# Optimization experiments

Hardware: AMD Instinct MI355X
Metric: run time of the kernel (lower is better)

Reference implementation:

```python
import jax, jax.numpy as jnp
import numpy as np

D_MODEL, SEQ, D_HEAD, N_HEAD, D_MLP = 1024, 2048, 64, 16, 4096
BATCH = 2
LN_EPS = 1e-5


def layer_norm(x, gamma, beta):
    mu = jnp.mean(x, axis=-1, keepdims=True)
    var = jnp.mean(jnp.square(x - mu), axis=-1, keepdims=True)
    return (x - mu) * jax.lax.rsqrt(var + LN_EPS) * gamma + beta


def setup_inputs() -> dict:
    key = jax.random.key(0)
    ks = jax.random.split(key, 10)
    s = 1.0 / np.sqrt(D_MODEL)
    x = jax.random.normal(ks[0], (BATCH, SEQ, D_MODEL), dtype=jnp.float32)
    # per-head Q/K/V projections, stacked: [H, d_model, d_head]
    wq = jax.random.uniform(ks[1], (N_HEAD, D_MODEL, D_HEAD), jnp.float32, -s, s)
    wk = jax.random.uniform(ks[2], (N_HEAD, D_MODEL, D_HEAD), jnp.float32, -s, s)
    wv = jax.random.uniform(ks[3], (N_HEAD, D_MODEL, D_HEAD), jnp.float32, -s, s)
    wo = jax.random.uniform(ks[4], (N_HEAD * D_HEAD, D_MODEL), jnp.float32, -s, s)
    sm = 1.0 / np.sqrt(D_MLP)
    w_in = jax.random.uniform(ks[5], (D_MODEL, D_MLP), jnp.float32, -s, s)
    b_in = jax.random.uniform(ks[6], (D_MLP,), jnp.float32, -s, s)
    w_out = jax.random.uniform(ks[7], (D_MLP, D_MODEL), jnp.float32, -sm, sm)
    b_out = jax.random.uniform(ks[8], (D_MODEL,), jnp.float32, -sm, sm)
    g1 = jnp.ones((D_MODEL,), jnp.float32)
    bt1 = jnp.zeros((D_MODEL,), jnp.float32)
    g2 = jnp.ones((D_MODEL,), jnp.float32)
    bt2 = jnp.zeros((D_MODEL,), jnp.float32)
    return {"x": x, "wq": wq, "wk": wk, "wv": wv, "wo": wo,
            "w_in": w_in, "b_in": b_in, "w_out": w_out, "b_out": b_out,
            "g1": g1, "bt1": bt1, "g2": g2, "bt2": bt2}


def reference(x, wq, wk, wv, wo, w_in, b_in, w_out, b_out, g1, bt1, g2, bt2):
    B, S, D = x.shape
    # multi-head attention (all heads batched)
    q = jnp.einsum('bsd,hde->bhse', x, wq)  # [B,H,S,dh]
    k = jnp.einsum('bsd,hde->bhse', x, wk)
    v = jnp.einsum('bsd,hde->bhse', x, wv)
    scores = jnp.einsum('bhie,bhje->bhij', q, k) / np.sqrt(D_HEAD)
    causal = jnp.tril(jnp.ones((S, S), dtype=bool))
    scores = jnp.where(causal, scores, -jnp.inf)
    attn = jax.nn.softmax(scores, axis=-1)
    head_out = jnp.einsum('bhij,bhje->bhie', attn, v)  # [B,H,S,dh]
    # concat heads in order (head 0 first) -> [B,S,H*dh]
    head_out = jnp.transpose(head_out, (0, 2, 1, 3)).reshape(B, S, N_HEAD * D_HEAD)
    x = x + layer_norm(head_out @ wo, g1, bt1)
    mlp = jax.nn.relu(x @ w_in + b_in) @ w_out + b_out
    x = x + layer_norm(mlp, g2, bt2)
    return x
```

## Files before the change

kernel.cpp:

```cpp
#include <hip/hip_runtime.h>
#include <hip/hip_bf16.h>
#include <math.h>

#define DM 1024
#define SEQ 2048
#define DH 64
#define NH 16
#define DMLP 4096
#define BATCH 2
#define ROWS (BATCH*SEQ)

typedef __attribute__((ext_vector_type(4))) float f32x4;
typedef __attribute__((ext_vector_type(8))) short bf16x8;

__device__ __forceinline__ void gl2lds16(const __hip_bfloat16* g, __hip_bfloat16* l) {
  __builtin_amdgcn_global_load_lds(
      (const __attribute__((address_space(1))) void*)g,
      (__attribute__((address_space(3))) void*)l, 16, 0, 0);
}

__device__ __forceinline__ float bfu2f(unsigned short u) {
  union { unsigned int i; float f; } cvt;
  cvt.i = ((unsigned int)u) << 16;
  return cvt.f;
}

template<int K, int OUT_BF16, int BIAS, int RELU>
__global__ __launch_bounds__(512) void gemm256(
    const __hip_bfloat16* __restrict__ A,
    const __hip_bfloat16* __restrict__ BT,
    float* __restrict__ Cf,
    __hip_bfloat16* __restrict__ Cb,
    const float* __restrict__ bias,
    int N)
{
  constexpr int NT = K / 64;
  __shared__ __align__(16) __hip_bfloat16 As[2][16384];
  __shared__ __align__(16) __hip_bfloat16 Bs[2][16384];
  const int t    = threadIdx.x;
  const int wave = t >> 6;
  const int lane = t & 63;
  const int col  = lane & 15;
  const int quad = lane >> 4;
  const int m0 = blockIdx.x * 256;
  const int n0 = blockIdx.y * 256;
  const int wm = (wave >> 2) * 128;
  const int wn = (wave & 3) * 64;

  const int tr = t >> 3;
  const int tc = (t & 7) ^ (tr & 7);
  const __hip_bfloat16* gA = A  + (size_t)(m0 + tr) * K + tc * 8;
  const __hip_bfloat16* gB = BT + (size_t)(n0 + tr) * K + tc * 8;

  const int sw  = col & 7;
  const int ao0 = ((quad)     ^ sw) * 8;
  const int ao1 = ((4 + quad) ^ sw) * 8;

  f32x4 acc[8][4] = {};

#define STAGE_A(h, u) do {                                                     \
    gl2lds16(gA + (size_t)(h)*128*K + (u)*64,                                  \
             &As[(u)&1][(h)*8192 + wave*512]);                                 \
    gl2lds16(gA + (size_t)(h)*128*K + (u)*64 + (size_t)64*K,                   \
             &As[(u)&1][(h)*8192 + 4096 + wave*512]);                          \
  } while (0)
#define STAGE_B(h, u) do {                                                     \
    gl2lds16(gB + (size_t)(h)*128*K + (u)*64,                                  \
             &Bs[(u)&1][(h)*8192 + wave*512]);                                 \
    gl2lds16(gB + (size_t)(h)*128*K + (u)*64 + (size_t)64*K,                   \
             &Bs[(u)&1][(h)*8192 + 4096 + wave*512]);                          \
  } while (0)
#define LOAD_A(base) do { _Pragma("unroll")                                    \
    for (int i = 0; i < 4; ++i) {                                              \
      af[i][0] = *(const bf16x8*)(pA + (base) + i*1024 + ao0);                 \
      af[i][1] = *(const bf16x8*)(pA + (base) + i*1024 + ao1);                 \
    } } while (0)
#define LOAD_BX(arr, base) do { _Pragma("unroll")                              \
    for (int j = 0; j < 2; ++j) {                                              \
      arr[j][0] = *(const bf16x8*)(pB + (base) + j*1024 + ao0);                \
      arr[j][1] = *(const bf16x8*)(pB + (base) + j*1024 + ao1);                \
    } } while (0)
#define PHASE_TAIL(MB, NB, BARR) do {                                          \
    asm volatile("s_barrier" ::: "memory");                                    \
    asm volatile("s_waitcnt lgkmcnt(0)" ::: "memory");                         \
    __builtin_amdgcn_s_setprio(1);                                             \
    _Pragma("unroll")                                                          \
    for (int kk = 0; kk < 2; ++kk)                                             \
      _Pragma("unroll")                                                        \
      for (int i = 0; i < 4; ++i)                                              \
        _Pragma("unroll")                                                      \
        for (int j = 0; j < 2; ++j)                                            \
          acc[(MB)+i][(NB)+j] = __builtin_amdgcn_mfma_f32_16x16x32_bf16(       \
              af[i][kk], BARR[j][kk], acc[(MB)+i][(NB)+j], 0, 0, 0);           \
    __builtin_amdgcn_s_setprio(0);                                             \
    asm volatile("s_barrier" ::: "memory");                                    \
  } while (0)

  STAGE_A(0, 0); STAGE_B(0, 0); STAGE_A(1, 0); STAGE_B(1, 0);
  if (NT > 1) {
    STAGE_A(0, 1); STAGE_B(0, 1); STAGE_A(1, 1); STAGE_B(1, 1);
    asm volatile("s_waitcnt vmcnt(8)" ::: "memory");
  } else {
    asm volatile("s_waitcnt vmcnt(0)" ::: "memory");
  }
  asm volatile("s_barrier" ::: "memory");

  #pragma unroll 2
  for (int u = 0; u < NT; ++u) {
    const __hip_bfloat16* pA = As[u & 1] + (wm + col) * 64;
    const __hip_bfloat16* pB = Bs[u & 1] + (wn + col) * 64;
    const bool s2 = (u + 2 < NT);
    bf16x8 af[4][2], bl[2][2], bh[2][2];

    LOAD_A(0);
    LOAD_BX(bl, 0);
    PHASE_TAIL(0, 0, bl);

    LOAD_BX(bh, 2048);
    PHASE_TAIL(0, 2, bh);

    LOAD_A(4096);
    if (s2) { STAGE_B(0, u + 2); STAGE_B(1, u + 2); }
    PHASE_TAIL(4, 2, bh);

    if (s2) {
      STAGE_A(0, u + 2); STAGE_A(1, u + 2);
      asm volatile("s_waitcnt vmcnt(8)" ::: "memory");
    } else {
      asm volatile("s_waitcnt vmcnt(0)" ::: "memory");
    }
    PHASE_TAIL(4, 0, bl);
  }
#undef STAGE_A
#undef STAGE_B
#undef LOAD_A
#undef LOAD_BX
#undef PHASE_TAIL

  #pragma unroll
  for (int mi = 0; mi < 8; ++mi) {
    #pragma unroll
    for (int ni = 0; ni < 4; ++ni) {
      const int cn = n0 + wn + ni*16 + col;
      float bv = 0.f;
      if (BIAS) bv = bias[cn];
      #pragma unroll
      for (int r = 0; r < 4; ++r) {
        const int cm = m0 + wm + mi*16 + quad*4 + r;
        float v = acc[mi][ni][r];
        if (BIAS) v += bv;
        if (RELU) v = fmaxf(v, 0.f);
        if (OUT_BF16) Cb[(size_t)cm * N + cn] = __float2bfloat16(v);
        else          Cf[(size_t)cm * N + cn] = v;
      }
    }
  }
}

template<int KS>
__global__ __launch_bounds__(512) void gemm256x128(
    const __hip_bfloat16* __restrict__ A,
    const __hip_bfloat16* __restrict__ BT,
    float* __restrict__ Cf,
    int N, int K, long long zstride)
{
  constexpr int NT = KS / 64;
  static_assert(NT >= 2, "pipeline needs >=2 K-tiles");
  __shared__ __align__(16) __hip_bfloat16 As[2][16384];
  __shared__ __align__(16) __hip_bfloat16 Bs[2][8192];
  const int t    = threadIdx.x;
  const int wave = t >> 6;
  const int lane = t & 63;
  const int col  = lane & 15;
  const int quad = lane >> 4;
  const int m0 = blockIdx.x * 256;
  const int n0 = blockIdx.y * 128;
  const int kz = (int)blockIdx.z * KS;
  const int wm = (wave >> 1) * 64;
  const int wn = (wave & 1) * 64;

  const int tr = t >> 3;
  const int tc = (t & 7) ^ (tr & 7);
  const __hip_bfloat16* gA = A  + (size_t)(m0 + tr) * K + kz + tc * 8;
  const __hip_bfloat16* gB = BT + (size_t)(n0 + tr) * K + kz + tc * 8;

  const int sw  = col & 7;
  const int ao0 = ((quad)     ^ sw) * 8;
  const int ao1 = ((4 + quad) ^ sw) * 8;

  f32x4 acc[4][4] = {};

#define SA(u) do { _Pragma("unroll")                                           \
    for (int q = 0; q < 4; ++q)                                                \
      gl2lds16(gA + (size_t)(q*64)*K + (u)*64,                                 \
               &As[(u)&1][q*4096 + wave*512]);                                 \
  } while (0)
#define SB(u) do { _Pragma("unroll")                                           \
    for (int q = 0; q < 2; ++q)                                                \
      gl2lds16(gB + (size_t)(q*64)*K + (u)*64,                                 \
               &Bs[(u)&1][q*4096 + wave*512]);                                 \
  } while (0)

  SA(0); SB(0); SA(1);

  #pragma unroll 2
  for (int v = 0; v < NT; ++v) {
    const __hip_bfloat16* pA = As[v & 1] + (wm + col) * 64;
    const __hip_bfloat16* pB = Bs[v & 1] + (wn + col) * 64;
    bf16x8 af[4][2], bf[4][2];

    if (v + 1 < NT) {
      SB(v + 1);
      asm volatile("s_waitcnt vmcnt(6)" ::: "memory");
    } else {
      asm volatile("s_waitcnt vmcnt(0)" ::: "memory");
    }
    asm volatile("s_barrier" ::: "memory");
    #pragma unroll
    for (int i = 0; i < 4; ++i) {
      af[i][0] = *(const bf16x8*)(pA + i*1024 + ao0);
      af[i][1] = *(const bf16x8*)(pA + i*1024 + ao1);
    }
    #pragma unroll
    for (int j = 0; j < 2; ++j) {
      bf[j][0] = *(const bf16x8*)(pB + j*1024 + ao0);
      bf[j][1] = *(const bf16x8*)(pB + j*1024 + ao1);
    }
    asm volatile("s_waitcnt lgkmcnt(0)" ::: "memory");
    __builtin_amdgcn_s_setprio(1);
    #pragma unroll
    for (int kk = 0; kk < 2; ++kk)
      #pragma unroll
      for (int i = 0; i < 4; ++i)
        #pragma unroll
        for (int j = 0; j < 2; ++j)
          acc[i][j] = __builtin_amdgcn_mfma_f32_16x16x32_bf16(
              af[i][kk], bf[j][kk], acc[i][j], 0, 0, 0);
    __builtin_amdgcn_s_setprio(0);
    asm volatile("s_barrier" ::: "memory");

    if (v + 2 < NT) SA(v + 2);
    #pragma unroll
    for (int j = 2; j < 4; ++j) {
      bf[j][0] = *(const bf16x8*)(pB + j*1024 + ao0);
      bf[j][1] = *(const bf16x8*)(pB + j*1024 + ao1);
    }
    asm volatile("s_waitcnt lgkmcnt(0)" ::: "memory");
    __builtin_amdgcn_s_setprio(1);
    #pragma unroll
    for (int kk = 0; kk < 2; ++kk)
      #pragma unroll
      for (int i = 0; i < 4; ++i)
        #pragma unroll
        for (int j = 2; j < 4; ++j)
          acc[i][j] = __builtin_amdgcn_mfma_f32_16x16x32_bf16(
              af[i][kk], bf[j][kk], acc[i][j], 0, 0, 0);
    __builtin_amdgcn_s_setprio(0);
    asm volatile("s_barrier" ::: "memory");
  }
#undef SA
#undef SB

  float* Co = Cf + (size_t)blockIdx.z * zstride;
  #pragma unroll
  for (int i = 0; i < 4; ++i) {
    #pragma unroll
    for (int j = 0; j < 4; ++j) {
      const int cn = n0 + wn + j*16 + col;
      #pragma unroll
      for (int r = 0; r < 4; ++r) {
        const int cm = m0 + wm + i*16 + quad*4 + r;
        Co[(size_t)cm * N + cn] = acc[i][j][r];
      }
    }
  }
}

__global__ __launch_bounds__(256) void attn_kernel(
    const __hip_bfloat16* __restrict__ qkv,
    const __hip_bfloat16* __restrict__ vt,
    __hip_bfloat16* __restrict__ aout,
    __hip_bfloat16* __restrict__ opart,
    float* __restrict__ lpart)
{
  __shared__ __align__(16) __hip_bfloat16 Ks[2][64*64];
  __shared__ __align__(16) __hip_bfloat16 Vts[64*64];
  __shared__ __align__(16) __hip_bfloat16 Ps[4][16*64];

  const int bh = blockIdx.x, b = bh >> 4, h = bh & 15;
  const int t = threadIdx.x, wave = t >> 6, lane = t & 63;
  const int col = lane & 15, quad = lane >> 4;
  const float SC = 0.125f * 1.44269504f;

  const int r0  = t >> 3;
  const int cs0 = (t & 7) ^ (r0 & 7);
  const __hip_bfloat16* kbase = qkv + (size_t)b*SEQ*3072 + 1024 + h*64;
  const __hip_bfloat16* vbase = vt + (size_t)bh*64*SEQ;

#define KISSUE(j0, buf) do {                                                      \
    gl2lds16(kbase + (size_t)((j0) + r0)*3072      + cs0*8, &Ks[buf][wave*512]);  \
    gl2lds16(kbase + (size_t)((j0) + 32 + r0)*3072 + cs0*8, &Ks[buf][2048 + wave*512]); \
  } while (0)
#define VISSUE(j0) do {                                                           \
    gl2lds16(vbase + (size_t)r0*SEQ        + (j0) + cs0*8,  &Vts[wave*512]);      \
    gl2lds16(vbase + (size_t)(32 + r0)*SEQ + (j0) + cs0*8,  &Vts[2048 + wave*512]); \
  } while (0)

  const int y = (int)blockIdx.y;
  int c, tile;
  if (y < 32)      { c = 0; tile = 31 - y;  }
  else if (y < 56) { c = 1; tile = 63 - y;  }
  else if (y < 72) { c = 2; tile = 87 - y;  }
  else             { c = 3; tile = 103 - y; }
  const int jbeg = c * 8;
  const int jend = jbeg + min(8, tile + 1 - jbeg);

  const int i0 = tile * 64;
  const int i0w = i0 + wave*16;

  bf16x8 aq[2];
  #pragma unroll
  for (int kk = 0; kk < 2; kk++)
    aq[kk] = *(const bf16x8*)&qkv[((size_t)(b*SEQ + i0w + col))*3072 + h*64 + kk*32 + quad*8];

  f32x4 O[4] = {};
  float lsum[4] = {0.f, 0.f, 0.f, 0.f};

  KISSUE(jbeg * 64, 0);
  for (int jt = jbeg; jt < jend; jt++) {
    const int cur = (jt - jbeg) & 1;
    const int j0 = jt * 64;
    const bool pf = (jt + 1 < jend);
    asm volatile("s_barrier" ::: "memory");
    VISSUE(j0);
    if (pf) {
      KISSUE(j0 + 64, cur ^ 1);
      asm volatile("s_waitcnt vmcnt(4)" ::: "memory");
    } else {
      asm volatile("s_waitcnt vmcnt(2)" ::: "memory");
    }

    f32x4 S[4] = {};
    __builtin_amdgcn_s_setprio(1);
    #pragma unroll
    for (int kk = 0; kk < 2; kk++) {
      const int sl = ((kk*4 + quad) ^ (col & 7)) * 8;
      #pragma unroll
      for (int jl = 0; jl < 4; jl++) {
        bf16x8 bk = *(const bf16x8*)&Ks[cur][(jl*16 + col)*64 + sl];
        S[jl] = __builtin_amdgcn_mfma_f32_16x16x32_bf16(aq[kk], bk, S[jl], 0, 0, 0);
      }
    }
    __builtin_amdgcn_s_setprio(0);

    const bool diag = (jt == tile);
    #pragma unroll
    for (int r = 0; r < 4; r++) {
      const int row = quad*4 + r;
      const int ig = i0 + wave*16 + row;
      #pragma unroll
      for (int jl = 0; jl < 4; jl++) {
        float p = exp2f(S[jl][r] * SC);
        if (diag && (j0 + jl*16 + col > ig)) p = 0.f;
        lsum[r] += p;
        const int cc = jl*2 + (col >> 3);
        Ps[wave][row*64 + (cc ^ (row & 7))*8 + (col & 7)] = __float2bfloat16(p);
      }
    }

    if (pf) asm volatile("s_waitcnt vmcnt(2)" ::: "memory");
    else    asm volatile("s_waitcnt vmcnt(0)" ::: "memory");

    __builtin_amdgcn_s_setprio(1);
    #pragma unroll
    for (int kk = 0; kk < 2; kk++) {
      const int sl = ((kk*4 + quad) ^ (col & 7)) * 8;
      bf16x8 ap = *(const bf16x8*)&Ps[wave][col*64 + sl];
      #pragma unroll
      for (int et = 0; et < 4; et++) {
        bf16x8 bv = *(const bf16x8*)&Vts[(et*16 + col)*64 + sl];
        O[et] = __builtin_amdgcn_mfma_f32_16x16x32_bf16(ap, bv, O[et], 0, 0, 0);
      }
    }
    __builtin_amdgcn_s_setprio(0);
  }

  #pragma unroll
  for (int r = 0; r < 4; r++) {
    float s = lsum[r];
    s += __shfl_xor(s, 1);
    s += __shfl_xor(s, 2);
    s += __shfl_xor(s, 4);
    s += __shfl_xor(s, 8);
    const int m = b*SEQ + i0w + quad*4 + r;
    if (tile < 8) {
      const float inv = 1.f / s;
      #pragma unroll
      for (int et = 0; et < 4; et++)
        aout[(size_t)m*DM + h*64 + et*16 + col] = __float2bfloat16(O[et][r] * inv);
    } else {
      __hip_bfloat16* op = opart + ((size_t)c*ROWS + m)*DM + h*64;
      #pragma unroll
      for (int et = 0; et < 4; et++)
        op[et*16 + col] = __float2bfloat16(O[et][r]);
      if (col == 0) lpart[((size_t)c*ROWS + m)*16 + h] = s;
    }
  }
#undef KISSUE
#undef VISSUE
}

__global__ __launch_bounds__(256) void attn_finalize(
    const __hip_bfloat16* __restrict__ opart,
    const float* __restrict__ lpart,
    __hip_bfloat16* __restrict__ aout)
{
  const int y = blockIdx.x;
  const int b = y / 1536;
  const int rem = y % 1536;
  const int tile = 8 + (rem >> 6);
  const int rr = rem & 63;
  const int m = b*SEQ + tile*64 + rr;
  const int nch = (tile >> 3) + 1;
  const int tid = threadIdx.x;
  const int h = tid >> 4;
  float o0 = 0.f, o1 = 0.f, o2 = 0.f, o3 = 0.f, l = 0.f;
  for (int c = 0; c < nch; ++c) {
    const ushort4 v = ((const ushort4*)(opart + ((size_t)c*ROWS + m)*DM))[tid];
    o0 += bfu2f(v.x); o1 += bfu2f(v.y); o2 += bfu2f(v.z); o3 += bfu2f(v.w);
    l  += lpart[((size_t)c*ROWS + m)*16 + h];
  }
  const float inv = 1.f / l;
  __hip_bfloat16* p = aout + (size_t)m*DM + tid*4;
  p[0] = __float2bfloat16(o0 * inv);
  p[1] = __float2bfloat16(o1 * inv);
  p[2] = __float2bfloat16(o2 * inv);
  p[3] = __float2bfloat16(o3 * inv);
}

__global__ __launch_bounds__(256) void ln_res(
    const float* __restrict__ y0,
    const float* __restrict__ y1,
    const float* __restrict__ bias,
    const float* __restrict__ xres,
    float* __restrict__ xout,
    __hip_bfloat16* __restrict__ bout,
    const float* __restrict__ gamma,
    const float* __restrict__ beta)
{
  const int row = blockIdx.x;
  const int t = threadIdx.x;
  float4 v = ((const float4*)(y0 + (size_t)row*DM))[t];
  if (y1) {
    const float4 w = ((const float4*)(y1 + (size_t)row*DM))[t];
    v.x += w.x; v.y += w.y; v.z += w.z; v.w += w.w;
  }
  if (bias) {
    const float4 w = ((const float4*)bias)[t];
    v.x += w.x; v.y += w.y; v.z += w.z; v.w += w.w;
  }
  float s  = v.x + v.y + v.z + v.w;
  float sq = v.x*v.x + v.y*v.y + v.z*v.z + v.w*v.w;
  #pragma unroll
  for (int off = 32; off > 0; off >>= 1) {
    s  += __shfl_down(s, off);
    sq += __shfl_down(sq, off);
  }
  __shared__ float red[8];
  const int wave = t >> 6, lane = t & 63;
  if (lane == 0) { red[wave] = s; red[4 + wave] = sq; }
  __syncthreads();
  s  = red[0] + red[1] + red[2] + red[3];
  sq = red[4] + red[5] + red[6] + red[7];
  const float mu   = s * (1.f/DM);
  const float var  = sq * (1.f/DM) - mu*mu;
  const float rstd = rsqrtf(var + 1e-5f);
  const float4 g  = ((const float4*)gamma)[t];
  const float4 bt = ((const float4*)beta)[t];
  const float4 xr = ((const float4*)(xres + (size_t)row*DM))[t];
  float4 o;
  o.x = (v.x - mu)*rstd*g.x + bt.x + xr.x;
  o.y = (v.y - mu)*rstd*g.y + bt.y + xr.y;
  o.z = (v.z - mu)*rstd*g.z + bt.z + xr.z;
  o.w = (v.w - mu)*rstd*g.w + bt.w + xr.w;
  ((float4*)(xout + (size_t)row*DM))[t] = o;
  if (bout) {
    __hip_bfloat16* bp = bout + (size_t)row*DM + t*4;
    bp[0] = __float2bfloat16(o.x);
    bp[1] = __float2bfloat16(o.y);
    bp[2] = __float2bfloat16(o.z);
    bp[3] = __float2bfloat16(o.w);
  }
}

__global__ __launch_bounds__(256) void transpose_cvt(
    const float* __restrict__ src, __hip_bfloat16* __restrict__ dst,
    int K, int N, long long sz, long long dz)
{
  __shared__ float tile[32][33];
  const int z = blockIdx.z;
  const int k0 = blockIdx.y * 32, n0 = blockIdx.x * 32;
  const int tx = threadIdx.x & 31, ty = threadIdx.x >> 5;
  const float* s = src + (size_t)z*sz;
  __hip_bfloat16* d = dst + (size_t)z*dz;
  for (int i = ty; i < 32; i += 8)
    tile[i][tx] = s[(size_t)(k0+i)*N + n0 + tx];
  __syncthreads();
  for (int i = ty; i < 32; i += 8)
    d[(size_t)(n0+i)*K + k0 + tx] = __float2bfloat16(tile[tx][i]);
}

__global__ __launch_bounds__(256) void transpose_v(
    const __hip_bfloat16* __restrict__ qkv, __hip_bfloat16* __restrict__ vt)
{
  __shared__ __hip_bfloat16 tile[32][33];
  const int bh = blockIdx.z, b = bh >> 4, h = bh & 15;
  const int s0 = blockIdx.x * 32, e0 = blockIdx.y * 32;
  const int tx = threadIdx.x & 31, ty = threadIdx.x >> 5;
  for (int i = ty; i < 32; i += 8)
    tile[i][tx] = qkv[(size_t)(b*SEQ + s0+i)*3072 + 2048 + h*64 + e0 + tx];
  __syncthreads();
  for (int i = ty; i < 32; i += 8)
    vt[((size_t)bh*64 + e0+i)*SEQ + s0 + tx] = tile[tx][i];
}

__global__ __launch_bounds__(256) void cvt_bf16(
    const float* __restrict__ src, __hip_bfloat16* __restrict__ dst, int n4)
{
  const int i = blockIdx.x*256 + threadIdx.x;
  if (i < n4) {
    const float4 v = ((const float4*)src)[i];
    dst[i*4+0] = __float2bfloat16(v.x);
    dst[i*4+1] = __float2bfloat16(v.y);
    dst[i*4+2] = __float2bfloat16(v.z);
    dst[i*4+3] = __float2bfloat16(v.w);
  }
}

extern "C" void kernel_launch(void* const* d_in, const int* in_sizes, int n_in,
                              void* d_out, int out_size, void* d_ws, size_t ws_size,
                              hipStream_t stream)
{
  const float* x     = (const float*)d_in[0];
  const float* wq    = (const float*)d_in[1];
  const float* wk    = (const float*)d_in[2];
  const float* wv    = (const float*)d_in[3];
  const float* wo    = (const float*)d_in[4];
  const float* w_in  = (const float*)d_in[5];
  const float* b_in  = (const float*)d_in[6];
  const float* w_out = (const float*)d_in[7];
  const float* b_out = (const float*)d_in[8];
  const float* g1    = (const float*)d_in[9];
  const float* bt1   = (const float*)d_in[10];
  const float* g2    = (const float*)d_in[11];
  const float* bt2   = (const float*)d_in[12];
  float* out = (float*)d_out;

  char* ws = (char*)d_ws;
  __hip_bfloat16* xb     = (__hip_bfloat16*)(ws + 0);
  __hip_bfloat16* wqkvT  = (__hip_bfloat16*)(ws + 8388608);
  __hip_bfloat16* woT    = (__hip_bfloat16*)(ws + 14680064);
  __hip_bfloat16* w_inT  = (__hip_bfloat16*)(ws + 16777216);
  __hip_bfloat16* w_outT = (__hip_bfloat16*)(ws + 25165824);
  __hip_bfloat16* qkvb   = (__hip_bfloat16*)(ws + 33554432);
  __hip_bfloat16* vtb    = (__hip_bfloat16*)(ws + 58720256);
  __hip_bfloat16* attn_o = (__hip_bfloat16*)(ws + 0);
  __hip_bfloat16* opart  = (__hip_bfloat16*)(ws + 67108864);
  float*          lpart  = (float*)(ws + 100663296);
  float*          P0     = (float*)(ws + 33554432);
  float*          x1     = (float*)(ws + 75497472);
  __hip_bfloat16* x1b    = (__hip_bfloat16*)(ws + 92274688);
  __hip_bfloat16* hbuf   = (__hip_bfloat16*)(ws + 33554432);
  float*          M0     = (float*)(ws + 0);
  float*          M1     = (float*)(ws + 100663296);
  float*          P1     = (float*)(ws + 50331648);

  const long long PROJ_ZS = (long long)ROWS * DM;
  const long long MLP_ZS  = 100663296LL / 4;

  cvt_bf16<<<ROWS*DM/4/256, 256, 0, stream>>>(x, xb, ROWS*DM/4);

  transpose_cvt<<<dim3(2,32,16), 256, 0, stream>>>(wq, wqkvT,             DM, DH, (long long)DM*DH, (long long)DH*DM);
  transpose_cvt<<<dim3(2,32,16), 256, 0, stream>>>(wk, wqkvT + 1024*1024, DM, DH, (long long)DM*DH, (long long)DH*DM);
  transpose_cvt<<<dim3(2,32,16), 256, 0, stream>>>(wv, wqkvT + 2048*1024, DM, DH, (long long)DM*DH, (long long)DH*DM);
  transpose_cvt<<<dim3(32,32,1),  256, 0, stream>>>(wo,    woT,    DM,   DM,   0, 0);
  transpose_cvt<<<dim3(128,32,1), 256, 0, stream>>>(w_in,  w_inT,  DM,   DMLP, 0, 0);
  transpose_cvt<<<dim3(32,128,1), 256, 0, stream>>>(w_out, w_outT, DMLP, DM,   0, 0);

  gemm256<DM,1,0,0><<<dim3(ROWS/256, 3072/256), 512, 0, stream>>>(xb, wqkvT, nullptr, qkvb, nullptr, 3072);
  transpose_v<<<dim3(SEQ/32, 2, BATCH*NH), 256, 0, stream>>>(qkvb, vtb);
  attn_kernel<<<dim3(BATCH*NH, 80), 256, 0, stream>>>(qkvb, vtb, attn_o, opart, lpart);
  attn_finalize<<<3072, 256, 0, stream>>>(opart, lpart, attn_o);
  gemm256x128<512><<<dim3(ROWS/256, DM/128, 2), 512, 0, stream>>>(attn_o, woT, P0, DM, DM, PROJ_ZS);
  ln_res<<<ROWS, 256, 0, stream>>>(P0, P1, nullptr, x, x1, x1b, g1, bt1);
  gemm256<DM,1,1,1><<<dim3(ROWS/256, DMLP/256), 512, 0, stream>>>(x1b, w_inT, nullptr, hbuf, b_in, DMLP);
  gemm256x128<2048><<<dim3(ROWS/256, DM/128, 2), 512, 0, stream>>>(hbuf, w_outT, M0, DM, DMLP, MLP_ZS);
  ln_res<<<ROWS, 256, 0, stream>>>(M0, M1, b_out, x1, out, nullptr, g2, bt2);
}
```

Before: 238.0 us.

## Double-buffer V tiles in attention, split diagonal masking, use native exp2/rcp

The V tile now gets its own double buffer in LDS and is prefetched one iteration ahead along with K, instead of being loaded at the start of each iteration. This takes the V global load latency off the critical path between the QK^T and PV MFMAs, and the second wait is no longer needed. The softmax loop is split into a masked diagonal path and an unmasked path, and uses the hardware exp2 and rcp intrinsics. The cost is more LDS, which may lower occupancy, and slightly less precise exp and reciprocal.

```diff
diff --git a/kernel.cpp b/kernel.cpp
--- a/kernel.cpp
+++ b/kernel.cpp
@@ -284,7 +284,7 @@
     float* __restrict__ lpart)
 {
   __shared__ __align__(16) __hip_bfloat16 Ks[2][64*64];
-  __shared__ __align__(16) __hip_bfloat16 Vts[64*64];
+  __shared__ __align__(16) __hip_bfloat16 Vts[2][64*64];
   __shared__ __align__(16) __hip_bfloat16 Ps[4][16*64];
 
   const int bh = blockIdx.x, b = bh >> 4, h = bh & 15;
@@ -301,9 +301,9 @@
     gl2lds16(kbase + (size_t)((j0) + r0)*3072      + cs0*8, &Ks[buf][wave*512]);  \
     gl2lds16(kbase + (size_t)((j0) + 32 + r0)*3072 + cs0*8, &Ks[buf][2048 + wave*512]); \
   } while (0)
-#define VISSUE(j0) do {                                                           \
-    gl2lds16(vbase + (size_t)r0*SEQ        + (j0) + cs0*8,  &Vts[wave*512]);      \
-    gl2lds16(vbase + (size_t)(32 + r0)*SEQ + (j0) + cs0*8,  &Vts[2048 + wave*512]); \
+#define VISSUE(j0, buf) do {                                                      \
+    gl2lds16(vbase + (size_t)r0*SEQ        + (j0) + cs0*8,  &Vts[buf][wave*512]); \
+    gl2lds16(vbase + (size_t)(32 + r0)*SEQ + (j0) + cs0*8,  &Vts[buf][2048 + wave*512]); \
   } while (0)
 
   const int y = (int)blockIdx.y;
@@ -327,17 +327,18 @@
   float lsum[4] = {0.f, 0.f, 0.f, 0.f};
 
   KISSUE(jbeg * 64, 0);
+  VISSUE(jbeg * 64, 0);
   for (int jt = jbeg; jt < jend; jt++) {
     const int cur = (jt - jbeg) & 1;
     const int j0 = jt * 64;
     const bool pf = (jt + 1 < jend);
     asm volatile("s_barrier" ::: "memory");
-    VISSUE(j0);
     if (pf) {
       KISSUE(j0 + 64, cur ^ 1);
+      VISSUE(j0 + 64, cur ^ 1);
       asm volatile("s_waitcnt vmcnt(4)" ::: "memory");
     } else {
-      asm volatile("s_waitcnt vmcnt(2)" ::: "memory");
+      asm volatile("s_waitcnt vmcnt(0)" ::: "memory");
     }
 
     f32x4 S[4] = {};
@@ -353,23 +354,33 @@
     }
     __builtin_amdgcn_s_setprio(0);
 
-    const bool diag = (jt == tile);
-    #pragma unroll
-    for (int r = 0; r < 4; r++) {
-      const int row = quad*4 + r;
-      const int ig = i0 + wave*16 + row;
-      #pragma unroll
-      for (int jl = 0; jl < 4; jl++) {
-        float p = exp2f(S[jl][r] * SC);
-        if (diag && (j0 + jl*16 + col > ig)) p = 0.f;
-        lsum[r] += p;
-        const int cc = jl*2 + (col >> 3);
-        Ps[wave][row*64 + (cc ^ (row & 7))*8 + (col & 7)] = __float2bfloat16(p);
+    if (jt == tile) {
+      #pragma unroll
+      for (int r = 0; r < 4; r++) {
+        const int row = quad*4 + r;
+        const int ig = i0 + wave*16 + row;
+        #pragma unroll
+        for (int jl = 0; jl < 4; jl++) {
+          float p = __builtin_amdgcn_exp2f(S[jl][r] * SC);
+          if (j0 + jl*16 + col > ig) p = 0.f;
+          lsum[r] += p;
+          const int cc = jl*2 + (col >> 3);
+          Ps[wave][row*64 + (cc ^ (row & 7))*8 + (col & 7)] = __float2bfloat16(p);
+        }
       }
-    }
-
-    if (pf) asm volatile("s_waitcnt vmcnt(2)" ::: "memory");
-    else    asm volatile("s_waitcnt vmcnt(0)" ::: "memory");
+    } else {
+      #pragma unroll
+      for (int r = 0; r < 4; r++) {
+        const int row = quad*4 + r;
+        #pragma unroll
+        for (int jl = 0; jl < 4; jl++) {
+          float p = __builtin_amdgcn_exp2f(S[jl][r] * SC);
+          lsum[r] += p;
+          const int cc = jl*2 + (col >> 3);
+          Ps[wave][row*64 + (cc ^ (row & 7))*8 + (col & 7)] = __float2bfloat16(p);
+        }
+      }
+    }
 
     __builtin_amdgcn_s_setprio(1);
     #pragma unroll
@@ -378,7 +389,7 @@
       bf16x8 ap = *(const bf16x8*)&Ps[wave][col*64 + sl];
       #pragma unroll
       for (int et = 0; et < 4; et++) {
-        bf16x8 bv = *(const bf16x8*)&Vts[(et*16 + col)*64 + sl];
+        bf16x8 bv = *(const bf16x8*)&Vts[cur][(et*16 + col)*64 + sl];
         O[et] = __builtin_amdgcn_mfma_f32_16x16x32_bf16(ap, bv, O[et], 0, 0, 0);
       }
     }
@@ -394,7 +405,7 @@
     s += __shfl_xor(s, 8);
     const int m = b*SEQ + i0w + quad*4 + r;
     if (tile < 8) {
-      const float inv = 1.f / s;
+      const float inv = __builtin_amdgcn_rcpf(s);
       #pragma unroll
       for (int et = 0; et < 4; et++)
         aout[(size_t)m*DM + h*64 + et*16 + col] = __float2bfloat16(O[et][r] * inv);
@@ -430,7 +441,7 @@
     o0 += bfu2f(v.x); o1 += bfu2f(v.y); o2 += bfu2f(v.z); o3 += bfu2f(v.w);
     l  += lpart[((size_t)c*ROWS + m)*16 + h];
   }
-  const float inv = 1.f / l;
+  const float inv = __builtin_amdgcn_rcpf(l);
   __hip_bfloat16* p = aout + (size_t)m*DM + tid*4;
   p[0] = __float2bfloat16(o0 * inv);
   p[1] = __float2bfloat16(o1 * inv);
```

Result: no change. 233.5 us (-1.9%).
